# Optimization experiments

Hardware: AMD Instinct MI355X
Metric: run time of the kernel (lower is better)

Reference implementation:

```python
import jax, jax.numpy as jnp
import numpy as np

N_NODES = 50000
N_EDGES = 800000
N_GRAPHS = 512
IN_DIM, HID_DIM, LAT_DIM = 128, 128, 64


def _glorot(key, fan_in, fan_out):
    lim = np.sqrt(6.0 / (fan_in + fan_out))
    return jax.random.uniform(key, (fan_in, fan_out), jnp.float32, -lim, lim)


def gcn_conv(x, W, b, src, dst, deg_inv_sqrt):
    """PyG GCNConv: out = D^{-1/2}(A+I)D^{-1/2} x W + b (self-loops included)."""
    h = x @ W  # [N, F_out]
    norm = deg_inv_sqrt[src] * deg_inv_sqrt[dst]  # [E]
    msg = h[src] * norm[:, None]  # gather + scale, [E, F_out]
    out = jax.ops.segment_sum(msg, dst, num_segments=x.shape[0])  # scatter-add
    out = out + h * (deg_inv_sqrt * deg_inv_sqrt)[:, None]  # self-loop term
    return out + b


def setup_inputs() -> dict:
    key = jax.random.key(0)
    ks = jax.random.split(key, 12)
    x = jax.random.normal(ks[0], (N_NODES, IN_DIM), jnp.float32)
    edge_index = jax.random.randint(ks[1], (2, N_EDGES), 0, N_NODES, jnp.int64)
    batch = jnp.sort(jax.random.randint(ks[2], (N_NODES,), 0, N_GRAPHS, jnp.int64))
    return {
        "x": x,
        "edge_index": edge_index,
        "batch": batch,
        "W1": _glorot(ks[3], IN_DIM, HID_DIM), "b1": jnp.zeros((HID_DIM,), jnp.float32),
        "W2": _glorot(ks[4], HID_DIM, LAT_DIM), "b2": jnp.zeros((LAT_DIM,), jnp.float32),
        "W3": _glorot(ks[5], LAT_DIM, HID_DIM), "b3": jnp.zeros((HID_DIM,), jnp.float32),
        "W4": _glorot(ks[6], HID_DIM, IN_DIM), "b4": jnp.zeros((IN_DIM,), jnp.float32),
    }


def reference(x, edge_index, batch, W1, b1, W2, b2, W3, b3, W4, b4):
    n = x.shape[0]
    src, dst = edge_index[0], edge_index[1]
    # degrees with self-loops (PyG computes deg over col=dst, +1 for self-loop)
    deg = jax.ops.segment_sum(jnp.ones_like(dst, dtype=x.dtype), dst, num_segments=n) + 1.0
    dis = jax.lax.rsqrt(deg)
    # encoder
    h = jax.nn.relu(gcn_conv(x, W1, b1, src, dst, dis))
    z = gcn_conv(h, W2, b2, src, dst, dis)
    # scatter-mean pooling over graphs
    counts = jax.ops.segment_sum(jnp.ones((n,), x.dtype), batch, num_segments=N_GRAPHS)
    agg = jax.ops.segment_sum(z, batch, num_segments=N_GRAPHS) / jnp.maximum(counts, 1.0)[:, None]
    # decoder
    h2 = jax.nn.relu(gcn_conv(z, W3, b3, src, dst, dis))
    x_hat = gcn_conv(h2, W4, b4, src, dst, dis)
    return (x_hat, z, agg)
```

## Files before the change

### kernel.cpp

```cpp
#include <hip/hip_runtime.h>
#include <math.h>

#define N_NODES 50000
#define N_EDGES 800000
#define N_GRAPHS 512
#define CAP 62
#define NBINS 196
#define CAPB 5120
#define ABLK 4096
#define PROP_BLOCKS 2048
#define PROP_WAVES (PROP_BLOCKS * 4)
#define POOL_BLOCKS 512
#define P64_BLOCKS (PROP_BLOCKS - POOL_BLOCKS)

typedef unsigned short u16;
typedef unsigned int u32;
typedef __attribute__((ext_vector_type(8))) short bf16x8_t;
typedef __attribute__((ext_vector_type(4))) float f32x4_t;
typedef __attribute__((ext_vector_type(4))) unsigned int u32x4_t;

constexpr int NBLK_A = (N_EDGES + ABLK - 1) / ABLK;
constexpr int WCONV_TOT = 49152;
constexpr int NCW = (WCONV_TOT + 255) / 256;

__device__ __forceinline__ u16 f2bf(float f) {
    u32 u = __builtin_bit_cast(u32, f);
    return (u16)((u + 0x7fffu + ((u >> 16) & 1u)) >> 16);
}
__device__ __forceinline__ float bf2f(u16 s) {
    return __builtin_bit_cast(float, (u32)s << 16);
}
__device__ __forceinline__ float bf_lo(u32 u) { return __builtin_bit_cast(float, u << 16); }
__device__ __forceinline__ float bf_hi(u32 u) { return __builtin_bit_cast(float, u & 0xffff0000u); }

__device__ __forceinline__ bf16x8_t cvt8(const float* p) {
    float4 a = *reinterpret_cast<const float4*>(p);
    float4 b = *reinterpret_cast<const float4*>(p + 4);
    u32x4_t w;
    w.x = (u32)f2bf(a.x) | ((u32)f2bf(a.y) << 16);
    w.y = (u32)f2bf(a.z) | ((u32)f2bf(a.w) << 16);
    w.z = (u32)f2bf(b.x) | ((u32)f2bf(b.y) << 16);
    w.w = (u32)f2bf(b.z) | ((u32)f2bf(b.w) << 16);
    return __builtin_bit_cast(bf16x8_t, w);
}

__device__ __forceinline__ int block_exscan(int val, int* lds, int tid) {
    lds[tid] = val;
    __syncthreads();
#pragma unroll
    for (int off = 1; off < 256; off <<= 1) {
        int t = (tid >= off) ? lds[tid - off] : 0;
        __syncthreads();
        lds[tid] += t;
        __syncthreads();
    }
    return lds[tid] - val;
}

__global__ __launch_bounds__(256) void pre_scatter(const int* __restrict__ src,
                                                   const int* __restrict__ dst,
                                                   u32* __restrict__ binCnt,
                                                   u32* __restrict__ binList,
                                                   const float* __restrict__ W1, u16* __restrict__ wt1,
                                                   const float* __restrict__ W2, u16* __restrict__ wt2,
                                                   const float* __restrict__ W3, u16* __restrict__ wt3,
                                                   const float* __restrict__ W4, u16* __restrict__ wt4) {
    __shared__ int cur[256];
    __shared__ int lsStart[256];
    __shared__ int gbase[256];
    __shared__ int scanbuf[256];
    __shared__ u32 stage[ABLK];
    __shared__ int gpos[ABLK];
    int t = threadIdx.x;
    if (blockIdx.x >= NBLK_A) {
        int idx = (blockIdx.x - NBLK_A) * 256 + t;
        if (idx < WCONV_TOT) {
            const float* Wf;
            u16* Wt;
            int K, N, off;
            if (idx < 16384)      { Wf = W1; Wt = wt1; K = 128; N = 128; off = 0; }
            else if (idx < 24576) { Wf = W2; Wt = wt2; K = 128; N = 64;  off = 16384; }
            else if (idx < 32768) { Wf = W3; Wt = wt3; K = 64;  N = 128; off = 24576; }
            else                  { Wf = W4; Wt = wt4; K = 128; N = 128; off = 32768; }
            int q = idx - off;
            int k = q / N, n = q % N;
            Wt[n * K + k] = f2bf(Wf[q]);
        }
        return;
    }
    int e0 = blockIdx.x * ABLK;
    int nEdge = min(ABLK, N_EDGES - e0);

    cur[t] = 0;
    __syncthreads();

    int myBin[16], myRank[16];
    u32 myPack[16];
#pragma unroll
    for (int p = 0; p < 4; p++) {
        int off = p * 1024 + t * 4;
        bool ok = off < nEdge;
        int4 dv = ok ? *reinterpret_cast<const int4*>(dst + e0 + off) : make_int4(0, 0, 0, 0);
        int4 sv = ok ? *reinterpret_cast<const int4*>(src + e0 + off) : make_int4(0, 0, 0, 0);
        int ds[4] = {dv.x, dv.y, dv.z, dv.w};
        int ss[4] = {sv.x, sv.y, sv.z, sv.w};
#pragma unroll
        for (int j = 0; j < 4; j++) {
            int q = p * 4 + j;
            myBin[q] = ok ? (ds[j] >> 8) : -1;
            myPack[q] = (u32)(ss[j] & 0xFFFF) | ((u32)(ds[j] & 0xFF) << 16);
            myRank[q] = ok ? atomicAdd(&cur[ds[j] >> 8], 1) : 0;
        }
    }
    __syncthreads();
    int v = cur[t];
    int ex = block_exscan(v, scanbuf, t);
    lsStart[t] = ex;
    gbase[t] = (v > 0) ? (int)atomicAdd(&binCnt[t * 16], (u32)v) : 0;
    __syncthreads();
#pragma unroll
    for (int q = 0; q < 16; q++) {
        if (myBin[q] >= 0) {
            int idx = lsStart[myBin[q]] + myRank[q];
            int pq = gbase[myBin[q]] + myRank[q];
            stage[idx] = myPack[q];
            gpos[idx] = (pq < CAPB) ? (myBin[q] * CAPB + pq) : -1;
        }
    }
    __syncthreads();
    for (int i = t; i < nEdge; i += 256) {
        int pq = gpos[i];
        if (pq >= 0) binList[pq] = stage[i];
    }
}

__global__ __launch_bounds__(256) void bucket_build(const u32* __restrict__ binList,
                                                    const u32* __restrict__ binCnt,
                                                    u32* __restrict__ bucket,
                                                    float* __restrict__ dis) {
    __shared__ u32 rec[256 * 33];
    int b = blockIdx.x, t = threadIdx.x;
    for (int i = t; i < 256 * 33; i += 256) rec[i] = 0;
    __syncthreads();
    int ecnt = min((int)binCnt[b * 16], CAPB);
    const u32* lst = binList + (size_t)b * CAPB;
    u16* rec16 = reinterpret_cast<u16*>(rec);
    for (int i = t; i < ecnt; i += 256) {
        u32 pk = lst[i];
        int dlow = (pk >> 16) & 0xFF;
        int pos = (int)atomicAdd(&rec[dlow * 33], 1u);
        if (pos < CAP) rec16[dlow * 66 + 2 + pos] = (u16)(pk & 0xFFFF);
    }
    __syncthreads();
    int node0 = b * 256;
    int nNode = min(256, N_NODES - node0);
    for (int i = t; i < nNode * 32; i += 256)
        bucket[(size_t)node0 * 32 + i] = rec[(i >> 5) * 33 + (i & 31)];
    if (t < nNode) dis[node0 + t] = 1.0f / sqrtf((float)rec[t * 33] + 1.0f);
}

template <int N, int K, bool BIAS, bool RELU, bool SCALE, bool AF32>
__global__ __launch_bounds__(256) void gemm_mfma(const void* __restrict__ Avp,
                                                 const u16* __restrict__ Wt,
                                                 const float* __restrict__ bias,
                                                 const float* __restrict__ dis,
                                                 u16* __restrict__ C) {
    constexpr int KB = K / 32;
    constexpr int TN = N / 64;
    constexpr int TM = (N_NODES + 63) / 64;
    int wave = threadIdx.x >> 6;
    int lane = threadIdx.x & 63;
    int W = blockIdx.x * 4 + wave;
    if (W >= TM * TN) return;
    int tm = W / TN, tn = W % TN;
    int r16 = lane & 15;
    int kg = lane >> 4;

    bf16x8_t bf[4][KB];
#pragma unroll
    for (int nr = 0; nr < 4; nr++) {
        int colg = tn * 64 + nr * 16 + r16;
#pragma unroll
        for (int kb = 0; kb < KB; kb++)
            bf[nr][kb] = *reinterpret_cast<const bf16x8_t*>(Wt + (size_t)colg * K + kb * 32 + kg * 8);
    }

    f32x4_t acc[4][4];
#pragma unroll
    for (int mr = 0; mr < 4; mr++)
#pragma unroll
        for (int nr = 0; nr < 4; nr++)
#pragma unroll
            for (int t = 0; t < 4; t++) acc[mr][nr][t] = 0.f;

#pragma unroll
    for (int mr = 0; mr < 4; mr++) {
        int row = tm * 64 + mr * 16 + r16;
        if (row >= N_NODES) row = N_NODES - 1;
        bf16x8_t af[KB];
#pragma unroll
        for (int kb = 0; kb < KB; kb++) {
            if constexpr (AF32) {
                af[kb] = cvt8((const float*)Avp + (size_t)row * K + kb * 32 + kg * 8);
            } else {
                af[kb] = *reinterpret_cast<const bf16x8_t*>((const u16*)Avp + (size_t)row * K + kb * 32 + kg * 8);
            }
        }
#pragma unroll
        for (int kb = 0; kb < KB; kb++)
#pragma unroll
            for (int nr = 0; nr < 4; nr++)
                acc[mr][nr] = __builtin_amdgcn_mfma_f32_16x16x32_bf16(af[kb], bf[nr][kb],
                                                                      acc[mr][nr], 0, 0, 0);
    }

#pragma unroll
    for (int mr = 0; mr < 4; mr++) {
        float sc[4];
#pragma unroll
        for (int r = 0; r < 4; r++) {
            int row = tm * 64 + mr * 16 + kg * 4 + r;
            sc[r] = (SCALE && row < N_NODES) ? dis[row] : 1.f;
        }
#pragma unroll
        for (int nr = 0; nr < 4; nr++) {
            int colg = tn * 64 + nr * 16 + r16;
            float bv = BIAS ? bias[colg] : 0.f;
#pragma unroll
            for (int r = 0; r < 4; r++) {
                int row = tm * 64 + mr * 16 + kg * 4 + r;
                if (row < N_NODES) {
                    float v = acc[mr][nr][r] + bv;
                    if (RELU) v = fmaxf(v, 0.f);
                    if (SCALE) v *= sc[r];
                    C[(size_t)row * N + colg] = f2bf(v);
                }
            }
        }
    }
}

__global__ __launch_bounds__(256) void mlp2(const u16* __restrict__ t_in,
                                            const u16* __restrict__ wt3,
                                            const float* __restrict__ b3,
                                            const u16* __restrict__ wt4,
                                            const float* __restrict__ dis,
                                            u16* __restrict__ out) {
    __shared__ u16 h2s[64 * 128];
    char* h2b = reinterpret_cast<char*>(h2s);
    int wv = threadIdx.x >> 6;
    int lane = threadIdx.x & 63;
    int r16 = lane & 15;
    int kg = lane >> 4;
    int row0 = blockIdx.x * 64;

    {
        bf16x8_t bf[2][2];
#pragma unroll
        for (int nr = 0; nr < 2; nr++) {
            int colg = wv * 32 + nr * 16 + r16;
#pragma unroll
            for (int kb = 0; kb < 2; kb++)
                bf[nr][kb] = *reinterpret_cast<const bf16x8_t*>(wt3 + (size_t)colg * 64 + kb * 32 + kg * 8);
        }
        f32x4_t acc[4][2];
#pragma unroll
        for (int mr = 0; mr < 4; mr++)
#pragma unroll
            for (int nr = 0; nr < 2; nr++)
#pragma unroll
                for (int q = 0; q < 4; q++) acc[mr][nr][q] = 0.f;
#pragma unroll
        for (int mr = 0; mr < 4; mr++) {
            int row = row0 + mr * 16 + r16;
            if (row >= N_NODES) row = N_NODES - 1;
            bf16x8_t af[2];
#pragma unroll
            for (int kb = 0; kb < 2; kb++)
                af[kb] = *reinterpret_cast<const bf16x8_t*>(t_in + (size_t)row * 64 + kb * 32 + kg * 8);
#pragma unroll
            for (int kb = 0; kb < 2; kb++)
#pragma unroll
                for (int nr = 0; nr < 2; nr++)
                    acc[mr][nr] = __builtin_amdgcn_mfma_f32_16x16x32_bf16(af[kb], bf[nr][kb],
                                                                          acc[mr][nr], 0, 0, 0);
        }
#pragma unroll
        for (int mr = 0; mr < 4; mr++) {
#pragma unroll
            for (int nr = 0; nr < 2; nr++) {
                int colg = wv * 32 + nr * 16 + r16;
                float bv = b3[colg];
#pragma unroll
                for (int r = 0; r < 4; r++) {
                    int rowl = mr * 16 + kg * 4 + r;
                    float v = fmaxf(acc[mr][nr][r] + bv, 0.f);
                    int off = rowl * 256 + colg * 2;
                    *reinterpret_cast<u16*>(h2b + (off ^ ((rowl & 7) << 4))) = f2bf(v);
                }
            }
        }
    }
    __syncthreads();

    {
        bf16x8_t bf[2][4];
#pragma unroll
        for (int nr = 0; nr < 2; nr++) {
            int colg = wv * 32 + nr * 16 + r16;
#pragma unroll
            for (int kb = 0; kb < 4; kb++)
                bf[nr][kb] = *reinterpret_cast<const bf16x8_t*>(wt4 + (size_t)colg * 128 + kb * 32 + kg * 8);
        }
        f32x4_t acc[4][2];
#pragma unroll
        for (int mr = 0; mr < 4; mr++)
#pragma unroll
            for (int nr = 0; nr < 2; nr++)
#pragma unroll
                for (int q = 0; q < 4; q++) acc[mr][nr][q] = 0.f;
#pragma unroll
        for (int mr = 0; mr < 4; mr++) {
            int rowl = mr * 16 + r16;
            bf16x8_t af[4];
#pragma unroll
            for (int kb = 0; kb < 4; kb++) {
                int off = rowl * 256 + kb * 64 + kg * 16;
                af[kb] = *reinterpret_cast<const bf16x8_t*>(h2b + (off ^ ((rowl & 7) << 4)));
            }
#pragma unroll
            for (int kb = 0; kb < 4; kb++)
#pragma unroll
                for (int nr = 0; nr < 2; nr++)
                    acc[mr][nr] = __builtin_amdgcn_mfma_f32_16x16x32_bf16(af[kb], bf[nr][kb],
                                                                          acc[mr][nr], 0, 0, 0);
        }
#pragma unroll
        for (int mr = 0; mr < 4; mr++) {
            float sc[4];
#pragma unroll
            for (int r = 0; r < 4; r++) {
                int row = row0 + mr * 16 + kg * 4 + r;
                sc[r] = (row < N_NODES) ? dis[row] : 1.f;
            }
#pragma unroll
            for (int nr = 0; nr < 2; nr++) {
                int colg = wv * 32 + nr * 16 + r16;
#pragma unroll
                for (int r = 0; r < 4; r++) {
                    int row = row0 + mr * 16 + kg * 4 + r;
                    if (row < N_NODES)
                        out[(size_t)row * 128 + colg] = f2bf(acc[mr][nr][r] * sc[r]);
                }
            }
        }
    }
}

template <int F, bool RELU, bool BIAS, bool WF32, bool WBF16, bool SCALEOUT>
__device__ void prop_dev(const u16* __restrict__ h, const u32* __restrict__ bucket,
                         const float* __restrict__ dis, const float* __restrict__ bias,
                         float* __restrict__ out_f, u16* __restrict__ out_b,
                         int wid, int nwaves, int lane) {
    float2 bv2 = make_float2(0.f, 0.f);
    float bv1 = 0.f;
    if (BIAS) {
        if (F == 128) bv2 = reinterpret_cast<const float2*>(bias)[lane];
        else          bv1 = bias[lane];
    }
    for (int w = wid; w < N_NODES; w += nwaves) {
        const u32* bw = bucket + (size_t)w * 32;
        int deg = __builtin_amdgcn_readfirstlane(min((int)bw[0], CAP));
        const u16* slots = reinterpret_cast<const u16*>(bw) + 2;
        const u32* sw = reinterpret_cast<const u32*>(reinterpret_cast<const char*>(bw) + 4);
        float di = dis[w];

        if (F == 128) {
            const u32* hw = reinterpret_cast<const u32*>(h);
            float2 a0 = {0.f, 0.f}, a1 = {0.f, 0.f}, a2 = {0.f, 0.f}, a3 = {0.f, 0.f};
            int i = 0;
            for (; i + 16 <= deg; i += 16) {
                u32 cw[8], hv[16];
#pragma unroll
                for (int j = 0; j < 8; j++) cw[j] = sw[(i >> 1) + j];
#pragma unroll
                for (int j = 0; j < 8; j++) {
                    hv[2 * j]     = hw[(size_t)(cw[j] & 0xffffu) * 64 + lane];
                    hv[2 * j + 1] = hw[(size_t)(cw[j] >> 16) * 64 + lane];
                }
#pragma unroll
                for (int j = 0; j < 16; j++) {
                    float lo = bf_lo(hv[j]), hi = bf_hi(hv[j]);
                    if ((j & 3) == 0) { a0.x += lo; a0.y += hi; }
                    else if ((j & 3) == 1) { a1.x += lo; a1.y += hi; }
                    else if ((j & 3) == 2) { a2.x += lo; a2.y += hi; }
                    else { a3.x += lo; a3.y += hi; }
                }
            }
            for (; i + 8 <= deg; i += 8) {
                u32 cw[4], hv[8];
#pragma unroll
                for (int j = 0; j < 4; j++) cw[j] = sw[(i >> 1) + j];
#pragma unroll
                for (int j = 0; j < 4; j++) {
                    hv[2 * j]     = hw[(size_t)(cw[j] & 0xffffu) * 64 + lane];
                    hv[2 * j + 1] = hw[(size_t)(cw[j] >> 16) * 64 + lane];
                }
#pragma unroll
                for (int j = 0; j < 8; j++) {
                    float lo = bf_lo(hv[j]), hi = bf_hi(hv[j]);
                    if ((j & 3) == 0) { a0.x += lo; a0.y += hi; }
                    else if ((j & 3) == 1) { a1.x += lo; a1.y += hi; }
                    else if ((j & 3) == 2) { a2.x += lo; a2.y += hi; }
                    else { a3.x += lo; a3.y += hi; }
                }
            }
            for (; i < deg; i++) {
                u32 u = hw[(size_t)slots[i] * 64 + lane];
                a0.x += bf_lo(u);
                a0.y += bf_hi(u);
            }
            u32 su = hw[(size_t)w * 64 + lane];
            float ox = (a0.x + a1.x + a2.x + a3.x + bf_lo(su)) * di;
            float oy = (a0.y + a1.y + a2.y + a3.y + bf_hi(su)) * di;
            if (BIAS) { ox += bv2.x; oy += bv2.y; }
            if (RELU) { ox = fmaxf(ox, 0.f); oy = fmaxf(oy, 0.f); }
            if (WF32) {
                reinterpret_cast<float2*>(out_f + (size_t)w * 128)[lane] = make_float2(ox, oy);
            }
            if (WBF16) {
                float wx = SCALEOUT ? ox * di : ox;
                float wy = SCALEOUT ? oy * di : oy;
                u32 pk = (u32)f2bf(wx) | ((u32)f2bf(wy) << 16);
                reinterpret_cast<u32*>(out_b)[(size_t)w * 64 + lane] = pk;
            }
        } else {
            float a0 = 0.f, a1 = 0.f, a2 = 0.f, a3 = 0.f;
            int i = 0;
            for (; i + 16 <= deg; i += 16) {
                u32 cw[8];
                u16 hv[16];
#pragma unroll
                for (int j = 0; j < 8; j++) cw[j] = sw[(i >> 1) + j];
#pragma unroll
                for (int j = 0; j < 8; j++) {
                    hv[2 * j]     = h[(size_t)(cw[j] & 0xffffu) * 64 + lane];
                    hv[2 * j + 1] = h[(size_t)(cw[j] >> 16) * 64 + lane];
                }
#pragma unroll
                for (int j = 0; j < 16; j++) {
                    float v = bf2f(hv[j]);
                    if ((j & 3) == 0) a0 += v;
                    else if ((j & 3) == 1) a1 += v;
                    else if ((j & 3) == 2) a2 += v;
                    else a3 += v;
                }
            }
            for (; i + 8 <= deg; i += 8) {
                u32 cw[4];
                u16 hv[8];
#pragma unroll
                for (int j = 0; j < 4; j++) cw[j] = sw[(i >> 1) + j];
#pragma unroll
                for (int j = 0; j < 4; j++) {
                    hv[2 * j]     = h[(size_t)(cw[j] & 0xffffu) * 64 + lane];
                    hv[2 * j + 1] = h[(size_t)(cw[j] >> 16) * 64 + lane];
                }
#pragma unroll
                for (int j = 0; j < 8; j++) {
                    float v = bf2f(hv[j]);
                    if ((j & 3) == 0) a0 += v;
                    else if ((j & 3) == 1) a1 += v;
                    else if ((j & 3) == 2) a2 += v;
                    else a3 += v;
                }
            }
            for (; i < deg; i++) a0 += bf2f(h[(size_t)slots[i] * 64 + lane]);
            float o = (a0 + a1 + a2 + a3 + bf2f(h[(size_t)w * 64 + lane])) * di;
            if (BIAS) o += bv1;
            if (RELU) o = fmaxf(o, 0.f);
            if (WF32) out_f[(size_t)w * 64 + lane] = o;
            if (WBF16) out_b[(size_t)w * 64 + lane] = f2bf(SCALEOUT ? o * di : o);
        }
    }
}

template <int F, bool RELU, bool BIAS, bool WF32, bool WBF16, bool SCALEOUT>
__global__ __launch_bounds__(256) void propagate_k(const u16* __restrict__ h,
                                                   const u32* __restrict__ bucket,
                                                   const float* __restrict__ dis,
                                                   const float* __restrict__ bias,
                                                   float* __restrict__ out_f,
                                                   u16* __restrict__ out_b) {
    prop_dev<F, RELU, BIAS, WF32, WBF16, SCALEOUT>(h, bucket, dis, bias, out_f, out_b,
        (int)(blockIdx.x * 4 + (threadIdx.x >> 6)), PROP_WAVES, threadIdx.x & 63);
}

__global__ __launch_bounds__(256) void prop64_pool(const u16* __restrict__ h,
                                                   const u32* __restrict__ bucket,
                                                   const float* __restrict__ dis,
                                                   u16* __restrict__ out_b,
                                                   const float* __restrict__ z,
                                                   const int* __restrict__ batch,
                                                   float* __restrict__ agg) {
    int wave = threadIdx.x >> 6;
    int lane = threadIdx.x & 63;
    if (blockIdx.x >= P64_BLOCKS) {
        __shared__ float part[3][64];
        int g = blockIdx.x - P64_BLOCKS;
        int l = 0, hh = N_NODES;
        while (l < hh) { int m = (l + hh) >> 1; if (batch[m] < g) l = m + 1; else hh = m; }
        int s = l;
        hh = N_NODES;
        while (l < hh) { int m = (l + hh) >> 1; if (batch[m] < g + 1) l = m + 1; else hh = m; }
        int e = l;
        float acc[4] = {0.f, 0.f, 0.f, 0.f};
        int i = s + wave;
        for (; i + 28 < e; i += 32) {
            float v[8];
#pragma unroll
            for (int j = 0; j < 8; j++) v[j] = z[(size_t)(i + j * 4) * 64 + lane];
#pragma unroll
            for (int j = 0; j < 8; j++) acc[j & 3] += v[j];
        }
        for (; i < e; i += 4) acc[0] += z[(size_t)i * 64 + lane];
        float a = acc[0] + acc[1] + acc[2] + acc[3];
        if (wave) part[wave - 1][lane] = a;
        __syncthreads();
        if (wave == 0) {
            a += part[0][lane] + part[1][lane] + part[2][lane];
            agg[(size_t)g * 64 + lane] = a / fmaxf((float)(e - s), 1.0f);
        }
        return;
    }
    prop_dev<64, false, false, false, true, false>(h, bucket, dis, nullptr, nullptr, out_b,
        (int)(blockIdx.x * 4 + wave), P64_BLOCKS * 4, lane);
}

extern "C" void kernel_launch(void* const* d_in, const int* in_sizes, int n_in,
                              void* d_out, int out_size, void* d_ws, size_t ws_size,
                              hipStream_t stream) {
    const float* x   = (const float*)d_in[0];
    const int* eidx  = (const int*)d_in[1];
    const int* batch = (const int*)d_in[2];
    const float* W1  = (const float*)d_in[3];
    const float* b1  = (const float*)d_in[4];
    const float* W2  = (const float*)d_in[5];
    const float* b2  = (const float*)d_in[6];
    const float* W3  = (const float*)d_in[7];
    const float* b3  = (const float*)d_in[8];
    const float* W4  = (const float*)d_in[9];
    const float* b4  = (const float*)d_in[10];

    const int* src = eidx;
    const int* dst = eidx + N_EDGES;

    float* out_xhat = (float*)d_out;
    float* out_z    = out_xhat + (size_t)N_NODES * 128;
    float* out_agg  = out_z + (size_t)N_NODES * 64;

    char* p = (char*)d_ws;
    auto alloc = [&](size_t bytes) { char* r = p; p += (bytes + 255) & ~(size_t)255; return r; };
    u16* arena0 = (u16*)alloc((size_t)N_NODES * 128 * 2);
    u16* arena1 = (u16*)alloc((size_t)N_NODES * 128 * 2);
    u16* c1     = (u16*)alloc((size_t)N_NODES * 64 * 2);
    u16* c2     = (u16*)alloc((size_t)N_NODES * 64 * 2);
    u16* wt1    = (u16*)alloc(128 * 128 * 2);
    u16* wt2    = (u16*)alloc(128 * 64 * 2);
    u16* wt3    = (u16*)alloc(64 * 128 * 2);
    u16* wt4    = (u16*)alloc(128 * 128 * 2);
    u32* bucket = (u32*)alloc((size_t)N_NODES * 128);
    u32* binCnt = (u32*)alloc(NBINS * 16 * 4);
    u32* binList= (u32*)alloc((size_t)NBINS * CAPB * 4);
    float* dis  = (float*)alloc(N_NODES * 4);

    hipMemsetAsync(binCnt, 0, NBINS * 16 * 4, stream);
    pre_scatter<<<NBLK_A + NCW, 256, 0, stream>>>(src, dst, binCnt, binList,
                                                  W1, wt1, W2, wt2, W3, wt3, W4, wt4);
    bucket_build<<<NBINS, 256, 0, stream>>>(binList, binCnt, bucket, dis);

    const int G128 = ((N_NODES + 63) / 64 * 2 + 3) / 4;
    const int G64  = ((N_NODES + 63) / 64 * 1 + 3) / 4;
    const int TILES = (N_NODES + 63) / 64;

    gemm_mfma<128, 128, false, false, true, true><<<G128, 256, 0, stream>>>(
        x, wt1, nullptr, dis, arena1);
    propagate_k<128, true, true, false, true, false><<<PROP_BLOCKS, 256, 0, stream>>>(
        arena1, bucket, dis, b1, nullptr, arena0);
    gemm_mfma<64, 128, false, false, true, false><<<G64, 256, 0, stream>>>(
        arena0, wt2, nullptr, dis, c1);
    propagate_k<64, false, true, true, true, true><<<PROP_BLOCKS, 256, 0, stream>>>(
        c1, bucket, dis, b2, out_z, c2);
    prop64_pool<<<PROP_BLOCKS, 256, 0, stream>>>(c2, bucket, dis, c1, out_z, batch, out_agg);
    mlp2<<<TILES, 256, 0, stream>>>(c1, wt3, b3, wt4, dis, arena0);
    propagate_k<128, false, true, true, false, false><<<PROP_BLOCKS, 256, 0, stream>>>(
        arena0, bucket, dis, b4, out_xhat, nullptr);
}
```

Before: 225.4 us.

## Fuse first 128-wide propagation with the 128x64 GEMM in one kernel

```diff
diff --git a/kernel.cpp b/kernel.cpp
--- a/kernel.cpp
+++ b/kernel.cpp
@@ -496,6 +496,92 @@
         (int)(blockIdx.x * 4 + (threadIdx.x >> 6)), PROP_WAVES, threadIdx.x & 63);
 }
 
+__global__ __launch_bounds__(256) void prop128_gemm64(const u16* __restrict__ h,
+                                                      const u32* __restrict__ bucket,
+                                                      const float* __restrict__ dis,
+                                                      const float* __restrict__ b1,
+                                                      const u16* __restrict__ wt2,
+                                                      u16* __restrict__ c1out) {
+    __shared__ u32 W2s[64 * 64];
+    const u32* wt2u = reinterpret_cast<const u32*>(wt2);
+    int t = threadIdx.x;
+    for (int i = t; i < 4096; i += 256) {
+        int j = i >> 6, kk = i & 63;
+        W2s[kk * 64 + j] = wt2u[j * 64 + kk];
+    }
+    __syncthreads();
+    int wid = (int)(blockIdx.x * 4 + (t >> 6));
+    int lane = t & 63;
+    float2 bv2 = reinterpret_cast<const float2*>(b1)[lane];
+    const u32* hw = reinterpret_cast<const u32*>(h);
+
+    for (int w = wid; w < N_NODES; w += PROP_WAVES) {
+        const u32* bw = bucket + (size_t)w * 32;
+        int deg = __builtin_amdgcn_readfirstlane(min((int)bw[0], CAP));
+        const u16* slots = reinterpret_cast<const u16*>(bw) + 2;
+        const u32* sw = reinterpret_cast<const u32*>(reinterpret_cast<const char*>(bw) + 4);
+        float di = dis[w];
+
+        float2 a0 = {0.f, 0.f}, a1 = {0.f, 0.f}, a2 = {0.f, 0.f}, a3 = {0.f, 0.f};
+        int i = 0;
+        for (; i + 16 <= deg; i += 16) {
+            u32 cw[8], hv[16];
+#pragma unroll
+            for (int j = 0; j < 8; j++) cw[j] = sw[(i >> 1) + j];
+#pragma unroll
+            for (int j = 0; j < 8; j++) {
+                hv[2 * j]     = hw[(size_t)(cw[j] & 0xffffu) * 64 + lane];
+                hv[2 * j + 1] = hw[(size_t)(cw[j] >> 16) * 64 + lane];
+            }
+#pragma unroll
+            for (int j = 0; j < 16; j++) {
+                float lo = bf_lo(hv[j]), hi = bf_hi(hv[j]);
+                if ((j & 3) == 0) { a0.x += lo; a0.y += hi; }
+                else if ((j & 3) == 1) { a1.x += lo; a1.y += hi; }
+                else if ((j & 3) == 2) { a2.x += lo; a2.y += hi; }
+                else { a3.x += lo; a3.y += hi; }
+            }
+        }
+        for (; i + 8 <= deg; i += 8) {
+            u32 cw[4], hv[8];
+#pragma unroll
+            for (int j = 0; j < 4; j++) cw[j] = sw[(i >> 1) + j];
+#pragma unroll
+            for (int j = 0; j < 4; j++) {
+                hv[2 * j]     = hw[(size_t)(cw[j] & 0xffffu) * 64 + lane];
+                hv[2 * j + 1] = hw[(size_t)(cw[j] >> 16) * 64 + lane];
+            }
+#pragma unroll
+            for (int j = 0; j < 8; j++) {
+                float lo = bf_lo(hv[j]), hi = bf_hi(hv[j]);
+                if ((j & 3) == 0) { a0.x += lo; a0.y += hi; }
+                else if ((j & 3) == 1) { a1.x += lo; a1.y += hi; }
+                else if ((j & 3) == 2) { a2.x += lo; a2.y += hi; }
+                else { a3.x += lo; a3.y += hi; }
+            }
+        }
+        for (; i < deg; i++) {
+            u32 u = hw[(size_t)slots[i] * 64 + lane];
+            a0.x += bf_lo(u);
+            a0.y += bf_hi(u);
+        }
+        u32 su = hw[(size_t)w * 64 + lane];
+        float ox = fmaxf((a0.x + a1.x + a2.x + a3.x + bf_lo(su)) * di + bv2.x, 0.f);
+        float oy = fmaxf((a0.y + a1.y + a2.y + a3.y + bf_hi(su)) * di + bv2.y, 0.f);
+
+        float acc = 0.f;
+#pragma unroll
+        for (int kk = 0; kk < 64; kk++) {
+            float ha = __shfl(ox, kk);
+            float hb = __shfl(oy, kk);
+            u32 wp = W2s[kk * 64 + lane];
+            acc = fmaf(ha, bf_lo(wp), acc);
+            acc = fmaf(hb, bf_hi(wp), acc);
+        }
+        c1out[(size_t)w * 64 + lane] = f2bf(di * acc);
+    }
+}
+
 __global__ __launch_bounds__(256) void prop64_pool(const u16* __restrict__ h,
                                                    const u32* __restrict__ bucket,
                                                    const float* __restrict__ dis,
@@ -580,15 +666,11 @@
     bucket_build<<<NBINS, 256, 0, stream>>>(binList, binCnt, bucket, dis);
 
     const int G128 = ((N_NODES + 63) / 64 * 2 + 3) / 4;
-    const int G64  = ((N_NODES + 63) / 64 * 1 + 3) / 4;
     const int TILES = (N_NODES + 63) / 64;
 
     gemm_mfma<128, 128, false, false, true, true><<<G128, 256, 0, stream>>>(
         x, wt1, nullptr, dis, arena1);
-    propagate_k<128, true, true, false, true, false><<<PROP_BLOCKS, 256, 0, stream>>>(
-        arena1, bucket, dis, b1, nullptr, arena0);
-    gemm_mfma<64, 128, false, false, true, false><<<G64, 256, 0, stream>>>(
-        arena0, wt2, nullptr, dis, c1);
+    prop128_gemm64<<<PROP_BLOCKS, 256, 0, stream>>>(arena1, bucket, dis, b1, wt2, c1);
     propagate_k<64, false, true, true, true, true><<<PROP_BLOCKS, 256, 0, stream>>>(
         c1, bucket, dis, b2, out_z, c2);
     prop64_pool<<<PROP_BLOCKS, 256, 0, stream>>>(c2, bucket, dis, c1, out_z, batch, out_agg);
```

After: 314.1 us. 39.4% more time.
